# Optimization experiments

Hardware: AMD Instinct MI355X
Metric: run time of the kernel (lower is better)

The kernel has to match this reference:

```python
import jax, jax.numpy as jnp
import numpy as np

B, L, D, H, SPD = 16, 512, 768, 12, 5
DH = D // H
LN_EPS = 1e-5
CLAMP_MIN = 1e-6


def setup_inputs() -> dict:
    key = jax.random.key(0)
    ks = jax.random.split(key, 8)
    s = 1.0 / np.sqrt(D)
    return {
        "tgt": jax.random.normal(ks[0], (B, L, D), jnp.float32),
        "query_pos": jax.random.normal(ks[1], (B, L, D), jnp.float32),
        "pairwise_locs": jax.random.normal(ks[2], (B, L, L, SPD), jnp.float32),
        "Wq": jax.random.normal(ks[3], (D, D), jnp.float32) * s,
        "bq": jnp.zeros((D,), jnp.float32),
        "Wk": jax.random.normal(ks[4], (D, D), jnp.float32) * s,
        "bk": jnp.zeros((D,), jnp.float32),
        "Wv": jax.random.normal(ks[5], (D, D), jnp.float32) * s,
        "bv": jnp.zeros((D,), jnp.float32),
        "Wo": jax.random.normal(ks[6], (D, D), jnp.float32) * s,
        "bo": jnp.zeros((D,), jnp.float32),
        "Wloc": jax.random.normal(ks[7], (SPD, H), jnp.float32) * (1.0 / np.sqrt(SPD)),
        "bloc": jnp.zeros((H,), jnp.float32),
        "ln_g": jnp.ones((D,), jnp.float32),
        "ln_b": jnp.zeros((D,), jnp.float32),
    }


def _layer_norm(x, g, b):
    mu = jnp.mean(x, axis=-1, keepdims=True)
    var = jnp.mean(jnp.square(x - mu), axis=-1, keepdims=True)
    return g * (x - mu) * jax.lax.rsqrt(var + LN_EPS) + b


def reference(tgt, query_pos, pairwise_locs, Wq, bq, Wk, bk, Wv, bv, Wo, bo, Wloc, bloc, ln_g, ln_b):
    # forward_post path: q = k = tgt + query_pos; v = tgt
    qk_in = tgt + query_pos
    q = (qk_in @ Wq + bq).reshape(B, L, H, DH)   # [B,L,H,DH]
    k = (qk_in @ Wk + bk).reshape(B, L, H, DH)
    v = (tgt @ Wv + bv).reshape(B, L, H, DH)

    scale = np.float32(1.0 / np.sqrt(DH))
    attn = jnp.einsum('blhd,bthd->bhlt', q, k) * scale   # [B,H,L,L]

    # spatial fusion 'mul': relu(Linear(pairwise_locs)) -> log-domain additive bias
    loc_attn = jax.nn.relu(pairwise_locs @ Wloc + bloc)   # [B,L,L,H]
    loc_attn = jnp.transpose(loc_attn, (0, 3, 1, 2))      # [B,H,L,L]
    fused = jax.nn.softmax(jnp.log(jnp.clip(loc_attn, CLAMP_MIN, None)) + attn, axis=-1)

    out = jnp.einsum('bhlt,bthd->blhd', fused, v).reshape(B, L, D)
    out = out @ Wo + bo                                   # attn output (tgt2)

    # residual + (dropout p=0) + LayerNorm
    return _layer_norm(tgt + out, ln_g, ln_b)
```

## Files before the change

kernel.cpp:

```cpp
#include <hip/hip_runtime.h>
#include <math.h>

#define BB 16
#define LL 512
#define DD 768
#define HH 12
#define DHH 64
#define SPDD 5
#define MM (BB*LL)
#define LN_EPS 1e-5f
#define CLAMP_MINV 1e-6f

typedef __attribute__((ext_vector_type(8))) short bf8_t;
typedef __attribute__((ext_vector_type(4))) float f4_t;

__device__ __forceinline__ short f2bf(float x) {
    unsigned u = __builtin_bit_cast(unsigned, x);
    unsigned r = (u + 0x7FFFu + ((u >> 16) & 1u)) >> 16;
    return (short)r;
}
__device__ __forceinline__ float bf2f(short s) {
    unsigned u = ((unsigned)(unsigned short)s) << 16;
    return __builtin_bit_cast(float, u);
}

__device__ __forceinline__ void gld16(const short* g, short* l) {
    __builtin_amdgcn_global_load_lds(
        (const __attribute__((address_space(1))) unsigned int*)g,
        (__attribute__((address_space(3))) unsigned int*)l,
        16, 0, 0);
}

__device__ __forceinline__ float block_sum(float v, float* red, int tid) {
    #pragma unroll
    for (int off = 32; off; off >>= 1) v += __shfl_down(v, off, 64);
    __syncthreads();
    if ((tid & 63) == 0) red[tid >> 6] = v;
    __syncthreads();
    return red[0] + red[1] + red[2] + red[3];
}

template<bool PRE>
__global__ __launch_bounds__(256) void prep_kernel(
    const float* __restrict__ tgt, const float* __restrict__ qpos,
    const float* __restrict__ ploc, const float* __restrict__ Wloc,
    const float* __restrict__ bloc,
    const float* __restrict__ W0, const float* __restrict__ W1,
    const float* __restrict__ W2, const float* __restrict__ W3,
    short* __restrict__ aqk, short* __restrict__ av, short* __restrict__ la,
    short* __restrict__ O0, short* __restrict__ O1,
    short* __restrict__ O2, short* __restrict__ O3)
{
    __shared__ float T[64][65];
    const int nbias = PRE ? 2048 : 0;
    const int t = blockIdx.x;
    if (PRE && t < nbias) {
        const int g   = t * 256 + threadIdx.x;
        const int tch = g & 63;
        const int l   = (g >> 6) & 511;
        const int b   = g >> 15;
        const int t0  = tch * 8;
        float p[40];
        const float* src = ploc + (((size_t)b * LL + l) * LL + t0) * SPDD;
        #pragma unroll
        for (int i = 0; i < 10; ++i)
            *(float4*)(p + i * 4) = *(const float4*)(src + i * 4);
        #pragma unroll
        for (int h = 0; h < HH; ++h) {
            float wl[SPDD];
            #pragma unroll
            for (int s = 0; s < SPDD; ++s) wl[s] = Wloc[s * HH + h];
            const float bl = bloc[h];
            short o[8];
            #pragma unroll
            for (int i = 0; i < 8; ++i) {
                float v = bl;
                #pragma unroll
                for (int s = 0; s < SPDD; ++s) v += p[i * SPDD + s] * wl[s];
                v = fmaxf(fmaxf(v, 0.f), CLAMP_MINV);
                o[i] = f2bf(v);
            }
            *(bf8_t*)(la + (((size_t)(b * HH + h) * LL + l) * LL + t0)) = *(bf8_t*)o;
        }
    } else if (t < nbias + 3072) {
        const int cb = t - nbias;
        const size_t base = ((size_t)cb * 256 + threadIdx.x) * 8;
        const float4 t0 = *(const float4*)(tgt + base);
        const float4 t1 = *(const float4*)(tgt + base + 4);
        const float4 p0 = *(const float4*)(qpos + base);
        const float4 p1 = *(const float4*)(qpos + base + 4);
        short v[8], q[8];
        v[0] = f2bf(t0.x); v[1] = f2bf(t0.y); v[2] = f2bf(t0.z); v[3] = f2bf(t0.w);
        v[4] = f2bf(t1.x); v[5] = f2bf(t1.y); v[6] = f2bf(t1.z); v[7] = f2bf(t1.w);
        q[0] = f2bf(t0.x + p0.x); q[1] = f2bf(t0.y + p0.y);
        q[2] = f2bf(t0.z + p0.z); q[3] = f2bf(t0.w + p0.w);
        q[4] = f2bf(t1.x + p1.x); q[5] = f2bf(t1.y + p1.y);
        q[6] = f2bf(t1.z + p1.z); q[7] = f2bf(t1.w + p1.w);
        *(bf8_t*)(av + base)  = *(bf8_t*)v;
        *(bf8_t*)(aqk + base) = *(bf8_t*)q;
    } else {
        const int wt = t - (nbias + 3072);
        const int wi = wt / 144;
        const int rem = wt % 144;
        const float* W; short* O;
        switch (wi) {
            case 0: W = W0; O = O0; break;
            case 1: W = W1; O = O1; break;
            case 2: W = W2; O = O2; break;
            default: W = W3; O = O3; break;
        }
        const int n0 = (rem % 12) * 64, k0 = (rem / 12) * 64;
        const int tid = threadIdx.x;
        {
            const int kk = tid >> 4, nv = (tid & 15) * 4;
            #pragma unroll
            for (int i = 0; i < 4; ++i) {
                const int k = kk + i * 16;
                const float4 v = *(const float4*)(W + (size_t)(k0 + k) * DD + n0 + nv);
                T[k][nv + 0] = v.x; T[k][nv + 1] = v.y;
                T[k][nv + 2] = v.z; T[k][nv + 3] = v.w;
            }
        }
        __syncthreads();
        {
            const int n = tid >> 2, kc = (tid & 3) * 16;
            short tmp[16];
            #pragma unroll
            for (int i = 0; i < 16; ++i) tmp[i] = f2bf(T[kc + i][n]);
            short* dst = O + (size_t)(n0 + n) * DD + k0 + kc;
            *(bf8_t*)dst       = *(bf8_t*)tmp;
            *(bf8_t*)(dst + 8) = *(bf8_t*)(tmp + 8);
        }
    }
}

__global__ __launch_bounds__(256) void gemm_qkv(
    const short* __restrict__ Aqk, const short* __restrict__ Av,
    const short* __restrict__ Wq, const float* __restrict__ bq, short* __restrict__ oq,
    const short* __restrict__ Wk, const float* __restrict__ bk, short* __restrict__ ok,
    const short* __restrict__ Wv, const float* __restrict__ bv, short* __restrict__ ov)
{
    __shared__ short As[128 * 64];
    __shared__ short Bs[128 * 64];
    const int id = blockIdx.y * 18 + blockIdx.x;
    const int xcd = id & 7, j = id >> 3;
    const int by = xcd * 8 + j / 18;
    const int gx = j % 18;
    const int seg = gx / 6;
    const int bx = gx % 6;
    const short* A  = (seg == 2) ? Av : Aqk;
    const short* Wt = (seg == 0) ? Wq : (seg == 1) ? Wk : Wv;
    const float* bias = (seg == 0) ? bq : (seg == 1) ? bk : bv;
    short* out = (seg == 0) ? oq : (seg == 1) ? ok : ov;

    const int n0 = bx * 128, m0 = by * 128;
    const int tid = threadIdx.x;
    const int w = tid >> 6, lane = tid & 63;
    const int quad = lane >> 4, l16 = lane & 15;
    const int wm = w & 1, wn = w >> 1;
    const int sr = w * 8 + (lane >> 3);
    const int sp = lane & 7;

    f4_t acc[4][4];
    #pragma unroll
    for (int i = 0; i < 4; ++i)
        #pragma unroll
        for (int jj = 0; jj < 4; ++jj) acc[i][jj] = (f4_t){0.f, 0.f, 0.f, 0.f};

    for (int k0 = 0; k0 < DD; k0 += 64) {
        __syncthreads();
        #pragma unroll
        for (int ra = 0; ra < 4; ++ra) {
            const int r = sr + ra * 32;
            const int c = sp ^ (r & 7);
            const int ldso = ra * 2048 + w * 512 + lane * 8;
            gld16(A  + (size_t)(m0 + r) * DD + k0 + c * 8, As + ldso);
            gld16(Wt + (size_t)(n0 + r) * DD + k0 + c * 8, Bs + ldso);
        }
        __syncthreads();
        #pragma unroll
        for (int s = 0; s < 2; ++s) {
            bf8_t a[4], b[4];
            #pragma unroll
            for (int i = 0; i < 4; ++i) {
                const int rA = wm * 64 + i * 16 + l16;
                const int pA = (s * 4 + quad) ^ (rA & 7);
                a[i] = *(const bf8_t*)(As + rA * 64 + pA * 8);
                const int rB = wn * 64 + i * 16 + l16;
                const int pB = (s * 4 + quad) ^ (rB & 7);
                b[i] = *(const bf8_t*)(Bs + rB * 64 + pB * 8);
            }
            #pragma unroll
            for (int i = 0; i < 4; ++i)
                #pragma unroll
                for (int jj = 0; jj < 4; ++jj)
                    acc[i][jj] = __builtin_amdgcn_mfma_f32_16x16x32_bf16(a[i], b[jj], acc[i][jj], 0, 0, 0);
        }
    }

    float bvv[4];
    #pragma unroll
    for (int jj = 0; jj < 4; ++jj) bvv[jj] = bias[n0 + wn * 64 + jj * 16 + l16];
    #pragma unroll
    for (int i = 0; i < 4; ++i) {
        #pragma unroll
        for (int jj = 0; jj < 4; ++jj) {
            const int n = n0 + wn * 64 + jj * 16 + l16;
            #pragma unroll
            for (int r = 0; r < 4; ++r) {
                const int m = m0 + wm * 64 + i * 16 + quad * 4 + r;
                const float val = acc[i][jj][r] + bvv[jj];
                const int b_ = m >> 9, l = m & 511;
                const int h = n >> 6, d = n & 63;
                if (seg < 2)
                    out[(((size_t)(b_ * HH + h)) * LL + l) * DHH + d] = f2bf(val);
                else
                    out[(((size_t)(b_ * HH + h)) * DHH + d) * LL + l] = f2bf(val);
            }
        }
    }
}

__global__ __launch_bounds__(256) void gemm_o(
    const short* __restrict__ A, const short* __restrict__ Wt,
    const float* __restrict__ bias, float* __restrict__ out)
{
    __shared__ short As[128 * 64];
    __shared__ short Bs[128 * 64];
    const int id = blockIdx.y * 6 + blockIdx.x;
    const int xcd = id & 7, j = id >> 3;
    const int by = xcd * 8 + j / 6;
    const int bx = j % 6;
    const int n0 = bx * 128, m0 = by * 128;
    const int tid = threadIdx.x;
    const int w = tid >> 6, lane = tid & 63;
    const int quad = lane >> 4, l16 = lane & 15;
    const int wm = w & 1, wn = w >> 1;
    const int sr = w * 8 + (lane >> 3);
    const int sp = lane & 7;

    f4_t acc[4][4];
    #pragma unroll
    for (int i = 0; i < 4; ++i)
        #pragma unroll
        for (int jj = 0; jj < 4; ++jj) acc[i][jj] = (f4_t){0.f, 0.f, 0.f, 0.f};

    for (int k0 = 0; k0 < DD; k0 += 64) {
        __syncthreads();
        #pragma unroll
        for (int ra = 0; ra < 4; ++ra) {
            const int r = sr + ra * 32;
            const int c = sp ^ (r & 7);
            const int ldso = ra * 2048 + w * 512 + lane * 8;
            gld16(A  + (size_t)(m0 + r) * DD + k0 + c * 8, As + ldso);
            gld16(Wt + (size_t)(n0 + r) * DD + k0 + c * 8, Bs + ldso);
        }
        __syncthreads();
        #pragma unroll
        for (int s = 0; s < 2; ++s) {
            bf8_t a[4], b[4];
            #pragma unroll
            for (int i = 0; i < 4; ++i) {
                const int rA = wm * 64 + i * 16 + l16;
                const int pA = (s * 4 + quad) ^ (rA & 7);
                a[i] = *(const bf8_t*)(As + rA * 64 + pA * 8);
                const int rB = wn * 64 + i * 16 + l16;
                const int pB = (s * 4 + quad) ^ (rB & 7);
                b[i] = *(const bf8_t*)(Bs + rB * 64 + pB * 8);
            }
            #pragma unroll
            for (int i = 0; i < 4; ++i)
                #pragma unroll
                for (int jj = 0; jj < 4; ++jj)
                    acc[i][jj] = __builtin_amdgcn_mfma_f32_16x16x32_bf16(a[i], b[jj], acc[i][jj], 0, 0, 0);
        }
    }

    float bvv[4];
    #pragma unroll
    for (int jj = 0; jj < 4; ++jj) bvv[jj] = bias[n0 + wn * 64 + jj * 16 + l16];
    #pragma unroll
    for (int i = 0; i < 4; ++i)
        #pragma unroll
        for (int jj = 0; jj < 4; ++jj) {
            const int n = n0 + wn * 64 + jj * 16 + l16;
            #pragma unroll
            for (int r = 0; r < 4; ++r) {
                const int m = m0 + wm * 64 + i * 16 + quad * 4 + r;
                out[(size_t)m * DD + n] = acc[i][jj][r] + bvv[jj];
            }
        }
}

template<bool PRE>
__global__ __launch_bounds__(256) void attn_mfma(
    const short* __restrict__ Q, const short* __restrict__ K,
    const short* __restrict__ Vt, const short* __restrict__ LA,
    const float* __restrict__ ploc, const float* __restrict__ Wloc,
    const float* __restrict__ bloc, short* __restrict__ out)
{
    __shared__ short Ks[64 * 64];
    __shared__ short Vs[64 * 64];
    __shared__ short bs16[64 * 68];
    __shared__ short Ps[4][16 * 64];

    const int h = blockIdx.x % 12, b = blockIdx.x / 12;
    const int qt = blockIdx.y;
    const int tid = threadIdx.x;
    const int w = tid >> 6, lane = tid & 63;
    const int quad = lane >> 4, l16 = lane & 15;
    const int q0 = qt * 64;
    const size_t bh = (size_t)b * HH + h;

    float wl[SPDD];
    float blc = 0.f;
    if (!PRE) {
        #pragma unroll
        for (int s = 0; s < SPDD; ++s) wl[s] = Wloc[s * HH + h];
        blc = bloc[h];
    }

    const int qr = q0 + w * 16 + l16;
    const bf8_t aq0 = *(const bf8_t*)(Q + (bh * LL + qr) * DHH + quad * 8);
    const bf8_t aq1 = *(const bf8_t*)(Q + (bh * LL + qr) * DHH + quad * 8 + 32);

    f4_t o[4];
    #pragma unroll
    for (int dj = 0; dj < 4; ++dj) o[dj] = (f4_t){0.f, 0.f, 0.f, 0.f};
    float m_row[4], l_row[4];
    #pragma unroll
    for (int r = 0; r < 4; ++r) { m_row[r] = -1e30f; l_row[r] = 0.f; }

    const short* Kg = K  + bh * LL * DHH;
    const short* Vg = Vt + bh * DHH * LL;
    const short* Bg = PRE ? (LA + (bh * LL + q0) * LL) : nullptr;

    const int srow = tid >> 2;
    const int cb   = (tid & 3) * 2;
    const int sw   = srow & 7;

    for (int t0 = 0; t0 < LL; t0 += 64) {
        __syncthreads();
        {
            const short* src = Kg + (size_t)(t0 + srow) * DHH + cb * 8;
            *(bf8_t*)(Ks + srow * 64 + ((cb ^ sw) * 8))       = *(const bf8_t*)(src);
            *(bf8_t*)(Ks + srow * 64 + (((cb + 1) ^ sw) * 8)) = *(const bf8_t*)(src + 8);
        }
        {
            const short* src = Vg + (size_t)srow * LL + t0 + cb * 8;
            *(bf8_t*)(Vs + srow * 64 + ((cb ^ sw) * 8))       = *(const bf8_t*)(src);
            *(bf8_t*)(Vs + srow * 64 + (((cb + 1) ^ sw) * 8)) = *(const bf8_t*)(src + 8);
        }
        {
            const int l = tid >> 2, ts = (tid & 3) * 16;
            if (PRE) {
                const short* src = Bg + (size_t)l * LL + t0 + ts;
                #pragma unroll
                for (int i = 0; i < 4; ++i)
                    *(short4*)(bs16 + l * 68 + ts + i * 4) = *(const short4*)(src + i * 4);
            } else {
                const float* pp = ploc + (((size_t)b * LL + q0 + l) * LL + t0 + ts) * SPDD;
                #pragma unroll
                for (int i = 0; i < 16; ++i) {
                    float v = blc;
                    #pragma unroll
                    for (int s = 0; s < SPDD; ++s) v += pp[i * SPDD + s] * wl[s];
                    v = fmaxf(fmaxf(v, 0.f), CLAMP_MINV);
                    bs16[l * 68 + ts + i] = f2bf(v);
                }
            }
        }
        __syncthreads();

        f4_t sv[4];
        #pragma unroll
        for (int j = 0; j < 4; ++j) {
            const int rB = j * 16 + l16;
            const int x = rB & 7;
            const bf8_t b0 = *(const bf8_t*)(Ks + rB * 64 + ((quad ^ x) * 8));
            const bf8_t b1 = *(const bf8_t*)(Ks + rB * 64 + (((quad + 4) ^ x) * 8));
            f4_t c = (f4_t){0.f, 0.f, 0.f, 0.f};
            c = __builtin_amdgcn_mfma_f32_16x16x32_bf16(aq0, b0, c, 0, 0, 0);
            c = __builtin_amdgcn_mfma_f32_16x16x32_bf16(aq1, b1, c, 0, 0, 0);
            sv[j] = c;
        }
        #pragma unroll
        for (int j = 0; j < 4; ++j)
            #pragma unroll
            for (int r = 0; r < 4; ++r) sv[j][r] *= 0.125f;

        #pragma unroll
        for (int r = 0; r < 4; ++r) {
            const int lrel = w * 16 + quad * 4 + r;
            float mx = fmaxf(fmaxf(sv[0][r], sv[1][r]), fmaxf(sv[2][r], sv[3][r]));
            mx = fmaxf(mx, __shfl_xor(mx, 1, 16));
            mx = fmaxf(mx, __shfl_xor(mx, 2, 16));
            mx = fmaxf(mx, __shfl_xor(mx, 4, 16));
            mx = fmaxf(mx, __shfl_xor(mx, 8, 16));
            const float mn = fmaxf(m_row[r], mx);
            const float al = __expf(m_row[r] - mn);
            m_row[r] = mn;
            float rs = 0.f;
            #pragma unroll
            for (int j = 0; j < 4; ++j) {
                const float lav = bf2f(bs16[lrel * 68 + j * 16 + l16]);
                const float p = lav * __expf(sv[j][r] - mn);
                sv[j][r] = p;
                rs += p;
            }
            rs += __shfl_xor(rs, 1, 16);
            rs += __shfl_xor(rs, 2, 16);
            rs += __shfl_xor(rs, 4, 16);
            rs += __shfl_xor(rs, 8, 16);
            l_row[r] = l_row[r] * al + rs;
            #pragma unroll
            for (int dj = 0; dj < 4; ++dj) o[dj][r] *= al;
        }
        short* Pw = Ps[w];
        #pragma unroll
        for (int r = 0; r < 4; ++r) {
            const int rp = quad * 4 + r, rp7 = rp & 7;
            #pragma unroll
            for (int j = 0; j < 4; ++j) {
                const int t = j * 16 + l16;
                Pw[rp * 64 + (((t >> 3) ^ rp7) * 8) + (t & 7)] = f2bf(sv[j][r]);
            }
        }
        const int m7 = l16 & 7;
        const bf8_t ap0 = *(const bf8_t*)(Pw + l16 * 64 + ((quad ^ m7) * 8));
        const bf8_t ap1 = *(const bf8_t*)(Pw + l16 * 64 + (((quad + 4) ^ m7) * 8));
        #pragma unroll
        for (int dj = 0; dj < 4; ++dj) {
            const int rB = dj * 16 + l16;
            const int x = rB & 7;
            const bf8_t b0 = *(const bf8_t*)(Vs + rB * 64 + ((quad ^ x) * 8));
            const bf8_t b1 = *(const bf8_t*)(Vs + rB * 64 + (((quad + 4) ^ x) * 8));
            o[dj] = __builtin_amdgcn_mfma_f32_16x16x32_bf16(ap0, b0, o[dj], 0, 0, 0);
            o[dj] = __builtin_amdgcn_mfma_f32_16x16x32_bf16(ap1, b1, o[dj], 0, 0, 0);
        }
    }

    #pragma unroll
    for (int r = 0; r < 4; ++r) {
        const int l = q0 + w * 16 + quad * 4 + r;
        const float inv = 1.f / l_row[r];
        short* op = out + ((size_t)b * LL + l) * DD + h * DHH;
        #pragma unroll
        for (int dj = 0; dj < 4; ++dj)
            op[dj * 16 + l16] = f2bf(o[dj][r] * inv);
    }
}

__global__ __launch_bounds__(256) void ln_kernel(
    const float* __restrict__ x, const float* __restrict__ tgt,
    const float* __restrict__ g, const float* __restrict__ bta,
    float* __restrict__ out)
{
    const int row = blockIdx.x;
    const int tid = threadIdx.x;
    __shared__ float red[4];

    const float* xp = x + (size_t)row * DD;
    const float* tp = tgt + (size_t)row * DD;

    float vals[3];
    float s = 0.f;
    #pragma unroll
    for (int i = 0; i < 3; ++i) {
        const float v = xp[tid + i * 256] + tp[tid + i * 256];
        vals[i] = v;
        s += v;
    }
    s = block_sum(s, red, tid);
    const float mu = s * (1.f / 768.f);

    float vs = 0.f;
    #pragma unroll
    for (int i = 0; i < 3; ++i) {
        const float dv = vals[i] - mu;
        vs += dv * dv;
    }
    vs = block_sum(vs, red, tid);
    const float rstd = rsqrtf(vs * (1.f / 768.f) + LN_EPS);

    #pragma unroll
    for (int i = 0; i < 3; ++i) {
        const int cidx = tid + i * 256;
        out[(size_t)row * DD + cidx] = g[cidx] * (vals[i] - mu) * rstd + bta[cidx];
    }
}

extern "C" void kernel_launch(void* const* d_in, const int* in_sizes, int n_in,
                              void* d_out, int out_size, void* d_ws, size_t ws_size,
                              hipStream_t stream) {
    const float* tgt   = (const float*)d_in[0];
    const float* qpos  = (const float*)d_in[1];
    const float* ploc  = (const float*)d_in[2];
    const float* Wq    = (const float*)d_in[3];
    const float* bq    = (const float*)d_in[4];
    const float* Wk    = (const float*)d_in[5];
    const float* bk    = (const float*)d_in[6];
    const float* Wv    = (const float*)d_in[7];
    const float* bv    = (const float*)d_in[8];
    const float* Wo    = (const float*)d_in[9];
    const float* bo    = (const float*)d_in[10];
    const float* Wloc  = (const float*)d_in[11];
    const float* bloc  = (const float*)d_in[12];
    const float* ln_g  = (const float*)d_in[13];
    const float* ln_b  = (const float*)d_in[14];

    const size_t NQ = (size_t)MM * DD;
    const size_t NW = (size_t)DD * DD;
    const size_t NB = (size_t)BB * HH * LL * LL;

    short* qb   = (short*)d_ws;
    short* kb   = qb  + NQ;
    short* vtb  = kb  + NQ;
    short* aob  = vtb + NQ;
    short* aqk  = aob + NQ;
    short* av   = aqk + NQ;
    float* pbuf = (float*)aqk;
    short* wqt  = av + NQ;
    short* wkt  = wqt + NW;
    short* wvt  = wkt + NW;
    short* wot  = wvt + NW;
    short* lab  = wot + NW;

    const size_t needed = (size_t)(6 * NQ + 4 * NW + NB) * 2;
    const bool pre = (ws_size >= needed);

    if (pre)
        prep_kernel<true ><<<5696, 256, 0, stream>>>(tgt, qpos, ploc, Wloc, bloc,
                                                     Wq, Wk, Wv, Wo,
                                                     aqk, av, lab, wqt, wkt, wvt, wot);
    else
        prep_kernel<false><<<3648, 256, 0, stream>>>(tgt, qpos, ploc, Wloc, bloc,
                                                     Wq, Wk, Wv, Wo,
                                                     aqk, av, lab, wqt, wkt, wvt, wot);

    gemm_qkv<<<dim3(18, 64), 256, 0, stream>>>(aqk, av, wqt, bq, qb,
                                               wkt, bk, kb, wvt, bv, vtb);

    if (pre)
        attn_mfma<true ><<<dim3(192, 8), 256, 0, stream>>>(qb, kb, vtb, lab, ploc, Wloc, bloc, aob);
    else
        attn_mfma<false><<<dim3(192, 8), 256, 0, stream>>>(qb, kb, vtb, nullptr, ploc, Wloc, bloc, aob);

    gemm_o<<<dim3(6, 64), 256, 0, stream>>>(aob, wot, bo, pbuf);

    ln_kernel<<<MM, 256, 0, stream>>>(pbuf, tgt, ln_g, ln_b, (float*)d_out);
}
```

Before: 368.4 us.

## Fuse location-bias computation into attention kernel with XCD-aware block remapping

```diff
diff --git a/kernel.cpp b/kernel.cpp
--- a/kernel.cpp
+++ b/kernel.cpp
@@ -40,51 +40,18 @@
     return red[0] + red[1] + red[2] + red[3];
 }
 
-template<bool PRE>
 __global__ __launch_bounds__(256) void prep_kernel(
     const float* __restrict__ tgt, const float* __restrict__ qpos,
-    const float* __restrict__ ploc, const float* __restrict__ Wloc,
-    const float* __restrict__ bloc,
     const float* __restrict__ W0, const float* __restrict__ W1,
     const float* __restrict__ W2, const float* __restrict__ W3,
-    short* __restrict__ aqk, short* __restrict__ av, short* __restrict__ la,
+    short* __restrict__ aqk, short* __restrict__ av,
     short* __restrict__ O0, short* __restrict__ O1,
     short* __restrict__ O2, short* __restrict__ O3)
 {
     __shared__ float T[64][65];
-    const int nbias = PRE ? 2048 : 0;
     const int t = blockIdx.x;
-    if (PRE && t < nbias) {
-        const int g   = t * 256 + threadIdx.x;
-        const int tch = g & 63;
-        const int l   = (g >> 6) & 511;
-        const int b   = g >> 15;
-        const int t0  = tch * 8;
-        float p[40];
-        const float* src = ploc + (((size_t)b * LL + l) * LL + t0) * SPDD;
-        #pragma unroll
-        for (int i = 0; i < 10; ++i)
-            *(float4*)(p + i * 4) = *(const float4*)(src + i * 4);
-        #pragma unroll
-        for (int h = 0; h < HH; ++h) {
-            float wl[SPDD];
-            #pragma unroll
-            for (int s = 0; s < SPDD; ++s) wl[s] = Wloc[s * HH + h];
-            const float bl = bloc[h];
-            short o[8];
-            #pragma unroll
-            for (int i = 0; i < 8; ++i) {
-                float v = bl;
-                #pragma unroll
-                for (int s = 0; s < SPDD; ++s) v += p[i * SPDD + s] * wl[s];
-                v = fmaxf(fmaxf(v, 0.f), CLAMP_MINV);
-                o[i] = f2bf(v);
-            }
-            *(bf8_t*)(la + (((size_t)(b * HH + h) * LL + l) * LL + t0)) = *(bf8_t*)o;
-        }
-    } else if (t < nbias + 3072) {
-        const int cb = t - nbias;
-        const size_t base = ((size_t)cb * 256 + threadIdx.x) * 8;
+    if (t < 3072) {
+        const size_t base = ((size_t)t * 256 + threadIdx.x) * 8;
         const float4 t0 = *(const float4*)(tgt + base);
         const float4 t1 = *(const float4*)(tgt + base + 4);
         const float4 p0 = *(const float4*)(qpos + base);
@@ -99,7 +66,7 @@
         *(bf8_t*)(av + base)  = *(bf8_t*)v;
         *(bf8_t*)(aqk + base) = *(bf8_t*)q;
     } else {
-        const int wt = t - (nbias + 3072);
+        const int wt = t - 3072;
         const int wi = wt / 144;
         const int rem = wt % 144;
         const float* W; short* O;
@@ -292,20 +259,23 @@
         }
 }
 
-template<bool PRE>
 __global__ __launch_bounds__(256) void attn_mfma(
     const short* __restrict__ Q, const short* __restrict__ K,
-    const short* __restrict__ Vt, const short* __restrict__ LA,
-    const float* __restrict__ ploc, const float* __restrict__ Wloc,
-    const float* __restrict__ bloc, short* __restrict__ out)
+    const short* __restrict__ Vt, const float* __restrict__ ploc,
+    const float* __restrict__ Wloc, const float* __restrict__ bloc,
+    short* __restrict__ out)
 {
     __shared__ short Ks[64 * 64];
     __shared__ short Vs[64 * 64];
     __shared__ short bs16[64 * 68];
     __shared__ short Ps[4][16 * 64];
 
-    const int h = blockIdx.x % 12, b = blockIdx.x / 12;
-    const int qt = blockIdx.y;
+    const int id = blockIdx.y * 12 + blockIdx.x;
+    const int xcd = id & 7, j = id >> 3;
+    const int pair = xcd * 16 + j / 12;
+    const int h = j % 12;
+    const int b = pair >> 3, qt = pair & 7;
+
     const int tid = threadIdx.x;
     const int w = tid >> 6, lane = tid & 63;
     const int quad = lane >> 4, l16 = lane & 15;
@@ -313,12 +283,9 @@
     const size_t bh = (size_t)b * HH + h;
 
     float wl[SPDD];
-    float blc = 0.f;
-    if (!PRE) {
-        #pragma unroll
-        for (int s = 0; s < SPDD; ++s) wl[s] = Wloc[s * HH + h];
-        blc = bloc[h];
-    }
+    #pragma unroll
+    for (int s = 0; s < SPDD; ++s) wl[s] = Wloc[s * HH + h];
+    const float blc = bloc[h];
 
     const int qr = q0 + w * 16 + l16;
     const bf8_t aq0 = *(const bf8_t*)(Q + (bh * LL + qr) * DHH + quad * 8);
@@ -333,11 +300,12 @@
 
     const short* Kg = K  + bh * LL * DHH;
     const short* Vg = Vt + bh * DHH * LL;
-    const short* Bg = PRE ? (LA + (bh * LL + q0) * LL) : nullptr;
 
     const int srow = tid >> 2;
     const int cb   = (tid & 3) * 2;
     const int sw   = srow & 7;
+    const int bl_l = tid >> 2, bl_ts = (tid & 3) * 16;
+    const float* plrow = ploc + (((size_t)b * LL + q0 + bl_l) * LL) * SPDD;
 
     for (int t0 = 0; t0 < LL; t0 += 64) {
         __syncthreads();
@@ -352,21 +320,20 @@
             *(bf8_t*)(Vs + srow * 64 + (((cb + 1) ^ sw) * 8)) = *(const bf8_t*)(src + 8);
         }
         {
-            const int l = tid >> 2, ts = (tid & 3) * 16;
-            if (PRE) {
-                const short* src = Bg + (size_t)l * LL + t0 + ts;
+            const float* pp = plrow + (size_t)(t0 + bl_ts) * SPDD;
+            #pragma unroll
+            for (int g4 = 0; g4 < 4; ++g4) {
+                float p[20];
                 #pragma unroll
-                for (int i = 0; i < 4; ++i)
-                    *(short4*)(bs16 + l * 68 + ts + i * 4) = *(const short4*)(src + i * 4);
-            } else {
-                const float* pp = ploc + (((size_t)b * LL + q0 + l) * LL + t0 + ts) * SPDD;
+                for (int c4 = 0; c4 < 5; ++c4)
+                    *(float4*)(p + c4 * 4) = *(const float4*)(pp + g4 * 20 + c4 * 4);
                 #pragma unroll
-                for (int i = 0; i < 16; ++i) {
+                for (int i = 0; i < 4; ++i) {
                     float v = blc;
                     #pragma unroll
-                    for (int s = 0; s < SPDD; ++s) v += pp[i * SPDD + s] * wl[s];
+                    for (int s = 0; s < SPDD; ++s) v += p[i * SPDD + s] * wl[s];
                     v = fmaxf(fmaxf(v, 0.f), CLAMP_MINV);
-                    bs16[l * 68 + ts + i] = f2bf(v);
+                    bs16[bl_l * 68 + bl_ts + g4 * 4 + i] = f2bf(v);
                 }
             }
         }
@@ -374,20 +341,20 @@
 
         f4_t sv[4];
         #pragma unroll
-        for (int j = 0; j < 4; ++j) {
-            const int rB = j * 16 + l16;
+        for (int j2 = 0; j2 < 4; ++j2) {
+            const int rB = j2 * 16 + l16;
             const int x = rB & 7;
             const bf8_t b0 = *(const bf8_t*)(Ks + rB * 64 + ((quad ^ x) * 8));
             const bf8_t b1 = *(const bf8_t*)(Ks + rB * 64 + (((quad + 4) ^ x) * 8));
             f4_t c = (f4_t){0.f, 0.f, 0.f, 0.f};
             c = __builtin_amdgcn_mfma_f32_16x16x32_bf16(aq0, b0, c, 0, 0, 0);
             c = __builtin_amdgcn_mfma_f32_16x16x32_bf16(aq1, b1, c, 0, 0, 0);
-            sv[j] = c;
-        }
-        #pragma unroll
-        for (int j = 0; j < 4; ++j)
-            #pragma unroll
-            for (int r = 0; r < 4; ++r) sv[j][r] *= 0.125f;
+            sv[j2] = c;
+        }
+        #pragma unroll
+        for (int j2 = 0; j2 < 4; ++j2)
+            #pragma unroll
+            for (int r = 0; r < 4; ++r) sv[j2][r] *= 0.125f;
 
         #pragma unroll
         for (int r = 0; r < 4; ++r) {
@@ -402,10 +369,10 @@
             m_row[r] = mn;
             float rs = 0.f;
             #pragma unroll
-            for (int j = 0; j < 4; ++j) {
-                const float lav = bf2f(bs16[lrel * 68 + j * 16 + l16]);
-                const float p = lav * __expf(sv[j][r] - mn);
-                sv[j][r] = p;
+            for (int j2 = 0; j2 < 4; ++j2) {
+                const float lav = bf2f(bs16[lrel * 68 + j2 * 16 + l16]);
+                const float p = lav * __expf(sv[j2][r] - mn);
+                sv[j2][r] = p;
                 rs += p;
             }
             rs += __shfl_xor(rs, 1, 16);
@@ -421,9 +388,9 @@
         for (int r = 0; r < 4; ++r) {
             const int rp = quad * 4 + r, rp7 = rp & 7;
             #pragma unroll
-            for (int j = 0; j < 4; ++j) {
-                const int t = j * 16 + l16;
-                Pw[rp * 64 + (((t >> 3) ^ rp7) * 8) + (t & 7)] = f2bf(sv[j][r]);
+            for (int j2 = 0; j2 < 4; ++j2) {
+                const int t = j2 * 16 + l16;
+                Pw[rp * 64 + (((t >> 3) ^ rp7) * 8) + (t & 7)] = f2bf(sv[j2][r]);
             }
         }
         const int m7 = l16 & 7;
@@ -511,7 +478,6 @@
 
     const size_t NQ = (size_t)MM * DD;
     const size_t NW = (size_t)DD * DD;
-    const size_t NB = (size_t)BB * HH * LL * LL;
 
     short* qb   = (short*)d_ws;
     short* kb   = qb  + NQ;
@@ -524,27 +490,14 @@
     short* wkt  = wqt + NW;
     short* wvt  = wkt + NW;
     short* wot  = wvt + NW;
-    short* lab  = wot + NW;
-
-    const size_t needed = (size_t)(6 * NQ + 4 * NW + NB) * 2;
-    const bool pre = (ws_size >= needed);
-
-    if (pre)
-        prep_kernel<true ><<<5696, 256, 0, stream>>>(tgt, qpos, ploc, Wloc, bloc,
-                                                     Wq, Wk, Wv, Wo,
-                                                     aqk, av, lab, wqt, wkt, wvt, wot);
-    else
-        prep_kernel<false><<<3648, 256, 0, stream>>>(tgt, qpos, ploc, Wloc, bloc,
-                                                     Wq, Wk, Wv, Wo,
-                                                     aqk, av, lab, wqt, wkt, wvt, wot);
+
+    prep_kernel<<<3648, 256, 0, stream>>>(tgt, qpos, Wq, Wk, Wv, Wo,
+                                          aqk, av, wqt, wkt, wvt, wot);
 
     gemm_qkv<<<dim3(18, 64), 256, 0, stream>>>(aqk, av, wqt, bq, qb,
                                                wkt, bk, kb, wvt, bv, vtb);
 
-    if (pre)
-        attn_mfma<true ><<<dim3(192, 8), 256, 0, stream>>>(qb, kb, vtb, lab, ploc, Wloc, bloc, aob);
-    else
-        attn_mfma<false><<<dim3(192, 8), 256, 0, stream>>>(qb, kb, vtb, nullptr, ploc, Wloc, bloc, aob);
+    attn_mfma<<<dim3(12, 128), 256, 0, stream>>>(qb, kb, vtb, ploc, Wloc, bloc, aob);
 
     gemm_o<<<dim3(6, 64), 256, 0, stream>>>(aob, wot, bo, pbuf);
 
```

Result: slower. 415.3 us (+12.8%).
